# Kernel tuning notes

Measured on AMD Instinct MI355X. Metric: run time of the kernel, lower is better.

Reference implementation:

```python
import jax, jax.numpy as jnp
import numpy as np

G, S, D = 2, 1024, 2048   # dispatch_group_size, seq_len_per_chip, hidden_dim
E, K = 8, 2               # num_routed_experts, num_experts_per_tok


def setup_inputs() -> dict:
    key = jax.random.key(0)
    ks = jax.random.split(key, 10)
    scale = 1.0 / np.sqrt(D)
    return {
        "x": jax.random.normal(ks[0], (G, S, D), jnp.float32),
        "weights": jax.random.uniform(ks[1], (G, S, K), jnp.float32),
        "indices": jax.random.randint(ks[2], (G, S, K), 0, E, jnp.int64),
        "expert_offsets": jnp.zeros((G, E), jnp.int64),
        "expert_token_counts": jnp.zeros((G, E), jnp.int64),
        # routed expert weights stacked over experts; F.linear(x, W) = x @ W.T, W is [out,in]=[D,D]
        "gate_w": jax.random.normal(ks[3], (E, D, D), jnp.float32) * scale,
        "up_w": jax.random.normal(ks[4], (E, D, D), jnp.float32) * scale,
        "down_w": jax.random.normal(ks[5], (E, D, D), jnp.float32) * scale,
        "shared_gate_w": jax.random.normal(ks[6], (D, D), jnp.float32) * scale,
        "shared_up_w": jax.random.normal(ks[7], (D, D), jnpp_dummy) if False else jax.random.normal(ks[7], (D, D), jnp.float32) * scale,
        "shared_down_w": jax.random.normal(ks[8], (D, D), jnp.float32) * scale,
    }


def expert_ffn(x, gw, uw, dw):
    # SiLU-gated FFN: silu(x @ gw.T) * (x @ uw.T) @ dw.T
    gate = jnp.einsum("gsd,od->gso", x, gw)
    up = jnp.einsum("gsd,od->gso", x, uw)
    act = jax.nn.silu(gate) * up
    return jnp.einsum("gsa,oa->gso", act, dw)


def reference(x, weights, indices, expert_offsets, expert_token_counts,
              gate_w, up_w, down_w, shared_gate_w, shared_up_w, shared_down_w):
    x = x.astype(jnp.float32)
    # shared expert on original tokens
    shared_out = expert_ffn(x, shared_gate_w, shared_up_w, shared_down_w)  # [G,S,D]

    # routed experts: compute all E expert FFNs densely (small E), then gather top-k
    gate = jnp.einsum("gsd,eod->egso", x, gate_w)      # [E,G,S,D]
    up = jnp.einsum("gsd,eod->egso", x, up_w)
    act = jax.nn.silu(gate) * up
    all_out = jnp.einsum("egsa,eoa->egso", act, down_w)  # [E,G,S,D]

    per_tok = jnp.transpose(all_out, (1, 2, 0, 3))       # [G,S,E,D]
    combined = jnp.take_along_axis(per_tok, indices[..., None], axis=2)  # [G,S,K,D]
    routed_out = jnp.sum(combined * weights[..., None], axis=2)          # [G,S,D]

    return routed_out + shared_out
```

## Files before the change

### kernel.cpp

```cpp
#include <hip/hip_runtime.h>
#include <cstdint>
#include <cstddef>

#define DHID 2048
#define NEXP 8
#define NTOK 2048
#define NPAIR 4096
#define NROWS 6144
#define MAXTILES 55
#define DD ((size_t)DHID * DHID)

typedef __attribute__((ext_vector_type(8))) __bf16 bf16x8;
typedef __attribute__((ext_vector_type(4))) __bf16 bf16x4;
typedef __attribute__((ext_vector_type(4))) float f32x4;

typedef __attribute__((address_space(3))) void lds_void;
typedef __attribute__((address_space(1))) void gbl_void;

__device__ __forceinline__ void gload16(const void* g, void* l) {
  __builtin_amdgcn_global_load_lds((gbl_void*)g, (lds_void*)l, 16, 0, 0);
}

__global__ void route_kernel(const int* __restrict__ idx, const float* __restrict__ wts,
                             int* __restrict__ tok_id, float* __restrict__ tok_w,
                             int* __restrict__ dst_id,
                             int* __restrict__ cnts, int* __restrict__ offs,
                             int2* __restrict__ tiles) {
  __shared__ int c[NEXP];
  __shared__ int cur[NEXP];
  const int t = threadIdx.x;
  if (t < NEXP) c[t] = 0;
  __syncthreads();
  for (int p = t; p < NPAIR; p += 256) atomicAdd(&c[idx[p]], 1);
  __syncthreads();
  if (t == 0) {
    int run = 0;
    for (int e = 0; e < NEXP; ++e) { cur[e] = run; offs[e] = run; cnts[e] = c[e]; run += c[e]; }
    offs[NEXP] = NPAIR; cnts[NEXP] = NTOK;
    int nt = 0;
    for (int e = 0; e <= NEXP; ++e) {
      const int ce = (e < NEXP) ? c[e] : NTOK;
      for (int m0 = 0; m0 < ce; m0 += 128) { tiles[nt].x = e; tiles[nt].y = m0; ++nt; }
    }
    for (; nt < MAXTILES; ++nt) { tiles[nt].x = -1; tiles[nt].y = 0; }
  }
  __syncthreads();
  for (int p = t; p < NPAIR; p += 256) {
    const int e = idx[p];
    const int slot = atomicAdd(&cur[e], 1);
    tok_id[slot] = p >> 1;
    tok_w[slot] = wts[p];
    dst_id[slot] = p;
  }
  for (int i = t; i < NTOK; i += 256) {
    tok_id[NPAIR + i] = i; tok_w[NPAIR + i] = 1.0f; dst_id[NPAIR + i] = NPAIR + i;
  }
}

__global__ void cast_all_kernel(const f32x4* __restrict__ gw, const f32x4* __restrict__ sgw,
                                const f32x4* __restrict__ uw, const f32x4* __restrict__ suw,
                                const f32x4* __restrict__ dwn, const f32x4* __restrict__ sdw,
                                const f32x4* __restrict__ x, bf16x4* __restrict__ dst) {
  const size_t L4 = DD / 4;
  const size_t base = (size_t)blockIdx.x * 512 + threadIdx.x;
#pragma unroll
  for (int half = 0; half < 2; ++half) {
    const size_t f = base + (size_t)half * 256;
    size_t r = f;
    const f32x4* src;
    if (r < 8 * L4) { src = gw; }
    else if ((r -= 8 * L4) < L4) { src = sgw; }
    else if ((r -= L4) < 8 * L4) { src = uw; }
    else if ((r -= 8 * L4) < L4) { src = suw; }
    else if ((r -= L4) < 8 * L4) { src = dwn; }
    else if ((r -= 8 * L4) < L4) { src = sdw; }
    else { r -= L4; src = x; }
    const f32x4 a = __builtin_nontemporal_load(src + r);
    bf16x4 o;
    o[0] = (__bf16)a[0]; o[1] = (__bf16)a[1]; o[2] = (__bf16)a[2]; o[3] = (__bf16)a[3];
    dst[f] = o;
  }
}

__global__ __launch_bounds__(256, 3) void gateup_kernel(
    const __bf16* __restrict__ xb,
    const __bf16* __restrict__ wbg, const __bf16* __restrict__ wbu,
    __bf16* __restrict__ act,
    const int* __restrict__ tok_id,
    const int* __restrict__ cnts, const int* __restrict__ offs,
    const int2* __restrict__ tiles) {
  const int2 tl = tiles[blockIdx.y];
  const int e = tl.x;
  if (e < 0) return;
  const int m0 = tl.y;
  const int cnt = cnts[e];
  const int n0 = blockIdx.x * 64;
  const int off = offs[e];
  const __bf16* Bg = wbg + (size_t)e * DD;
  const __bf16* Bu = wbu + (size_t)e * DD;

  __shared__ __align__(16) char sA[128 * 64 * 2];
  __shared__ __align__(16) char sBg[64 * 64 * 2];
  __shared__ __align__(16) char sBu[64 * 64 * 2];

  const int tid = threadIdx.x;
  const int lane = tid & 63;
  const int wv = tid >> 6;
  const int mw = (wv >> 1) * 64;
  const int nw = (wv & 1) * 32;
  const int q4 = lane >> 4;
  const int ln = lane & 15;

  const int rbase = tid >> 3;
  const int part = (tid & 7) ^ (rbase & 7);

  const char* gA[4];
#pragma unroll
  for (int j = 0; j < 4; ++j) {
    int r = m0 + rbase + 32 * j;
    r = (r < cnt) ? r : (cnt - 1);
    gA[j] = (const char*)(xb + (size_t)tok_id[off + r] * DHID) + part * 16;
  }
  const char* gBg[2]; const char* gBu[2];
#pragma unroll
  for (int j = 0; j < 2; ++j) {
    gBg[j] = (const char*)(Bg + (size_t)(n0 + rbase + 32 * j) * DHID) + part * 16;
    gBu[j] = (const char*)(Bu + (size_t)(n0 + rbase + 32 * j) * DHID) + part * 16;
  }

  f32x4 accg[4][2], accu[4][2];
  const f32x4 vz = {0.f, 0.f, 0.f, 0.f};
#pragma unroll
  for (int i = 0; i < 4; ++i)
#pragma unroll
    for (int j = 0; j < 2; ++j) { accg[i][j] = vz; accu[i][j] = vz; }

  for (int kt = 0; kt < DHID; kt += 64) {
#pragma unroll
    for (int j = 0; j < 4; ++j)
      gload16(gA[j] + (size_t)kt * 2, sA + (tid + j * 256) * 16);
#pragma unroll
    for (int j = 0; j < 2; ++j) {
      gload16(gBg[j] + (size_t)kt * 2, sBg + (tid + j * 256) * 16);
      gload16(gBu[j] + (size_t)kt * 2, sBu + (tid + j * 256) * 16);
    }
    __syncthreads();

#pragma unroll
    for (int h = 0; h < 2; ++h) {
      bf16x8 af[4];
#pragma unroll
      for (int im = 0; im < 4; ++im) {
        const int r = mw + im * 16 + ln;
        af[im] = *(const bf16x8*)(sA + ((r * 8 + ((q4 + 4 * h) ^ (r & 7))) << 4));
      }
#pragma unroll
      for (int in_ = 0; in_ < 2; ++in_) {
        const int r = nw + in_ * 16 + ln;
        const int c = (r * 8 + ((q4 + 4 * h) ^ (r & 7))) << 4;
        const bf16x8 bg = *(const bf16x8*)(sBg + c);
        const bf16x8 bu = *(const bf16x8*)(sBu + c);
#pragma unroll
        for (int im = 0; im < 4; ++im) {
          accg[im][in_] = __builtin_amdgcn_mfma_f32_16x16x32_bf16(af[im], bg, accg[im][in_], 0, 0, 0);
          accu[im][in_] = __builtin_amdgcn_mfma_f32_16x16x32_bf16(af[im], bu, accu[im][in_], 0, 0, 0);
        }
      }
    }
    __syncthreads();
  }

#pragma unroll
  for (int im = 0; im < 4; ++im) {
#pragma unroll
    for (int rr = 0; rr < 4; ++rr) {
      const int row = mw + im * 16 + q4 * 4 + rr;
      if (m0 + row < cnt) {
        __bf16* dst = act + (size_t)(off + m0 + row) * DHID + n0 + nw + ln;
#pragma unroll
        for (int in_ = 0; in_ < 2; ++in_) {
          const float gg = accg[im][in_][rr];
          const float uu = accu[im][in_][rr];
          const float a = (gg / (1.0f + __expf(-gg))) * uu;
          dst[in_ * 16] = (__bf16)a;
        }
      }
    }
  }
}

__global__ __launch_bounds__(256, 3) void down_kernel(
    const __bf16* __restrict__ act,
    const __bf16* __restrict__ wbd,
    float* __restrict__ buf,
    const float* __restrict__ tok_w, const int* __restrict__ dst_id,
    const int* __restrict__ cnts, const int* __restrict__ offs,
    const int2* __restrict__ tiles) {
  const int2 tl = tiles[blockIdx.y];
  const int e = tl.x;
  if (e < 0) return;
  const int m0 = tl.y;
  const int cnt = cnts[e];
  const int n0 = blockIdx.x * 128;
  const int off = offs[e];
  const __bf16* B = wbd + (size_t)e * DD;

  __shared__ __align__(16) char sA[128 * 64 * 2];
  __shared__ __align__(16) char sB[128 * 64 * 2];

  const int tid = threadIdx.x;
  const int lane = tid & 63;
  const int wv = tid >> 6;
  const int mw = (wv >> 1) * 64;
  const int nw = (wv & 1) * 64;
  const int q4 = lane >> 4;
  const int ln = lane & 15;

  const int rbase = tid >> 3;
  const int part = (tid & 7) ^ (rbase & 7);

  const char* gA[4];
  const char* gB[4];
#pragma unroll
  for (int j = 0; j < 4; ++j) {
    gA[j] = (const char*)(act + (size_t)(off + m0 + rbase + 32 * j) * DHID) + part * 16;
    gB[j] = (const char*)(B + (size_t)(n0 + rbase + 32 * j) * DHID) + part * 16;
  }

  f32x4 acc[4][4];
  const f32x4 vz = {0.f, 0.f, 0.f, 0.f};
#pragma unroll
  for (int i = 0; i < 4; ++i)
#pragma unroll
    for (int j = 0; j < 4; ++j) acc[i][j] = vz;

  for (int kt = 0; kt < DHID; kt += 64) {
#pragma unroll
    for (int j = 0; j < 4; ++j) {
      gload16(gA[j] + (size_t)kt * 2, sA + (tid + j * 256) * 16);
      gload16(gB[j] + (size_t)kt * 2, sB + (tid + j * 256) * 16);
    }
    __syncthreads();

#pragma unroll
    for (int h = 0; h < 2; ++h) {
      bf16x8 af[4], bfr[4];
#pragma unroll
      for (int im = 0; im < 4; ++im) {
        const int r = mw + im * 16 + ln;
        af[im] = *(const bf16x8*)(sA + ((r * 8 + ((q4 + 4 * h) ^ (r & 7))) << 4));
      }
#pragma unroll
      for (int in_ = 0; in_ < 4; ++in_) {
        const int r = nw + in_ * 16 + ln;
        bfr[in_] = *(const bf16x8*)(sB + ((r * 8 + ((q4 + 4 * h) ^ (r & 7))) << 4));
      }
#pragma unroll
      for (int in_ = 0; in_ < 4; ++in_)
#pragma unroll
        for (int im = 0; im < 4; ++im)
          acc[im][in_] = __builtin_amdgcn_mfma_f32_16x16x32_bf16(af[im], bfr[in_], acc[im][in_], 0, 0, 0);
    }
    __syncthreads();
  }

#pragma unroll
  for (int im = 0; im < 4; ++im) {
#pragma unroll
    for (int rr = 0; rr < 4; ++rr) {
      const int row = mw + im * 16 + q4 * 4 + rr;
      if (m0 + row < cnt) {
        const int gr = off + m0 + row;
        const float wt = tok_w[gr];
        float* dst = buf + (size_t)dst_id[gr] * DHID + n0 + nw + ln;
#pragma unroll
        for (int in_ = 0; in_ < 4; ++in_)
          dst[in_ * 16] = wt * acc[im][in_][rr];
      }
    }
  }
}

__global__ void combine_kernel(const float4* __restrict__ buf, float4* __restrict__ out) {
  const int i = blockIdx.x * 256 + threadIdx.x;
  const int t = i >> 9;
  const int d = i & 511;
  const float4 a = buf[(size_t)(2 * t) * 512 + d];
  const float4 b = buf[(size_t)(2 * t + 1) * 512 + d];
  const float4 c = buf[(size_t)(NPAIR + t) * 512 + d];
  float4 r;
  r.x = a.x + b.x + c.x; r.y = a.y + b.y + c.y;
  r.z = a.z + b.z + c.z; r.w = a.w + b.w + c.w;
  out[i] = r;
}

extern "C" void kernel_launch(void* const* d_in, const int* in_sizes, int n_in,
                              void* d_out, int out_size, void* d_ws, size_t ws_size,
                              hipStream_t stream) {
  (void)in_sizes; (void)n_in; (void)out_size; (void)ws_size;
  const float* x   = (const float*)d_in[0];
  const float* wts = (const float*)d_in[1];
  const int*   idx = (const int*)d_in[2];
  const float* gw  = (const float*)d_in[5];
  const float* uw  = (const float*)d_in[6];
  const float* dwn = (const float*)d_in[7];
  const float* sgw = (const float*)d_in[8];
  const float* suw = (const float*)d_in[9];
  const float* sdw = (const float*)d_in[10];
  float* out = (float*)d_out;
  char* ws = (char*)d_ws;

  const size_t WB    = 3 * 9 * DD * 2;
  const size_t XBsz  = (size_t)NTOK * DHID * 2;
  const size_t ACTsz = (size_t)NROWS * DHID * 2;
  const size_t BUFsz = (size_t)NROWS * DHID * 4;

  __bf16* wbg = (__bf16*)ws;
  __bf16* wbu = wbg + 9 * DD;
  __bf16* wbd = wbu + 9 * DD;
  __bf16* xb  = (__bf16*)(ws + WB);
  __bf16* act = (__bf16*)(ws + WB + XBsz);
  float*  buf = (float*)(ws + WB + XBsz + ACTsz);
  char*   rt  = ws + WB + XBsz + ACTsz + BUFsz;
  int*   tok_id = (int*)rt;
  float* tok_w  = (float*)(rt + NROWS * 4);
  int*   dst_id = (int*)(rt + NROWS * 8);
  int*   cnts   = (int*)(rt + NROWS * 12);
  int*   offs   = cnts + 16;
  int2*  tiles  = (int2*)(offs + 16);

  route_kernel<<<1, 256, 0, stream>>>(idx, wts, tok_id, tok_w, dst_id, cnts, offs, tiles);
  cast_all_kernel<<<57344, 256, 0, stream>>>((const f32x4*)gw, (const f32x4*)sgw,
                                             (const f32x4*)uw, (const f32x4*)suw,
                                             (const f32x4*)dwn, (const f32x4*)sdw,
                                             (const f32x4*)x, (bf16x4*)ws);
  gateup_kernel<<<dim3(32, MAXTILES), 256, 0, stream>>>(
      xb, wbg, wbu, act, tok_id, cnts, offs, tiles);
  down_kernel<<<dim3(16, MAXTILES), 256, 0, stream>>>(
      act, wbd, buf, tok_w, dst_id, cnts, offs, tiles);
  combine_kernel<<<4096, 256, 0, stream>>>((const float4*)buf, (float4*)out);
}
```

Baseline: 608.0 us.

## Fuse routing into cast kernel and overlap down-weight cast with gate/up GEMM

```diff
diff --git a/kernel.cpp b/kernel.cpp
--- a/kernel.cpp
+++ b/kernel.cpp
@@ -8,6 +8,7 @@
 #define NPAIR 4096
 #define NROWS 6144
 #define MAXTILES 55
+#define CASTY 144
 #define DD ((size_t)DHID * DHID)
 
 typedef __attribute__((ext_vector_type(8))) __bf16 bf16x8;
@@ -21,64 +22,64 @@
   __builtin_amdgcn_global_load_lds((gbl_void*)g, (lds_void*)l, 16, 0, 0);
 }
 
-__global__ void route_kernel(const int* __restrict__ idx, const float* __restrict__ wts,
-                             int* __restrict__ tok_id, float* __restrict__ tok_w,
-                             int* __restrict__ dst_id,
-                             int* __restrict__ cnts, int* __restrict__ offs,
-                             int2* __restrict__ tiles) {
-  __shared__ int c[NEXP];
-  __shared__ int cur[NEXP];
-  const int t = threadIdx.x;
-  if (t < NEXP) c[t] = 0;
-  __syncthreads();
-  for (int p = t; p < NPAIR; p += 256) atomicAdd(&c[idx[p]], 1);
-  __syncthreads();
-  if (t == 0) {
-    int run = 0;
-    for (int e = 0; e < NEXP; ++e) { cur[e] = run; offs[e] = run; cnts[e] = c[e]; run += c[e]; }
-    offs[NEXP] = NPAIR; cnts[NEXP] = NTOK;
-    int nt = 0;
-    for (int e = 0; e <= NEXP; ++e) {
-      const int ce = (e < NEXP) ? c[e] : NTOK;
-      for (int m0 = 0; m0 < ce; m0 += 128) { tiles[nt].x = e; tiles[nt].y = m0; ++nt; }
-    }
-    for (; nt < MAXTILES; ++nt) { tiles[nt].x = -1; tiles[nt].y = 0; }
-  }
-  __syncthreads();
-  for (int p = t; p < NPAIR; p += 256) {
-    const int e = idx[p];
-    const int slot = atomicAdd(&cur[e], 1);
-    tok_id[slot] = p >> 1;
-    tok_w[slot] = wts[p];
-    dst_id[slot] = p;
-  }
-  for (int i = t; i < NTOK; i += 256) {
-    tok_id[NPAIR + i] = i; tok_w[NPAIR + i] = 1.0f; dst_id[NPAIR + i] = NPAIR + i;
-  }
-}
-
-__global__ void cast_all_kernel(const f32x4* __restrict__ gw, const f32x4* __restrict__ sgw,
-                                const f32x4* __restrict__ uw, const f32x4* __restrict__ suw,
-                                const f32x4* __restrict__ dwn, const f32x4* __restrict__ sdw,
-                                const f32x4* __restrict__ x, bf16x4* __restrict__ dst) {
+__global__ void cast_route_kernel(
+    const f32x4* __restrict__ gw, const f32x4* __restrict__ sgw,
+    const f32x4* __restrict__ uw, const f32x4* __restrict__ suw,
+    const f32x4* __restrict__ x, bf16x4* __restrict__ dst,
+    const int* __restrict__ idx, const float* __restrict__ wts,
+    int* __restrict__ tok_id, float* __restrict__ tok_w,
+    int* __restrict__ dst_id,
+    int* __restrict__ cnts, int* __restrict__ offs,
+    int2* __restrict__ tiles) {
+  if (blockIdx.x == 0) {
+    __shared__ int c[NEXP];
+    __shared__ int cur[NEXP];
+    const int t = threadIdx.x;
+    if (t < NEXP) c[t] = 0;
+    __syncthreads();
+    for (int p = t; p < NPAIR; p += 256) atomicAdd(&c[idx[p]], 1);
+    __syncthreads();
+    if (t == 0) {
+      int run = 0;
+      for (int e = 0; e < NEXP; ++e) { cur[e] = run; offs[e] = run; cnts[e] = c[e]; run += c[e]; }
+      offs[NEXP] = NPAIR; cnts[NEXP] = NTOK;
+      int nt = 0;
+      for (int e = 0; e <= NEXP; ++e) {
+        const int ce = (e < NEXP) ? c[e] : NTOK;
+        for (int m0 = 0; m0 < ce; m0 += 128) { tiles[nt].x = e; tiles[nt].y = m0; ++nt; }
+      }
+      for (; nt < MAXTILES; ++nt) { tiles[nt].x = -1; tiles[nt].y = 0; }
+    }
+    __syncthreads();
+    for (int p = t; p < NPAIR; p += 256) {
+      const int e = idx[p];
+      const int slot = atomicAdd(&cur[e], 1);
+      tok_id[slot] = p >> 1;
+      tok_w[slot] = wts[p];
+      dst_id[slot] = p;
+    }
+    for (int i = t; i < NTOK; i += 256) {
+      tok_id[NPAIR + i] = i; tok_w[NPAIR + i] = 1.0f; dst_id[NPAIR + i] = NPAIR + i;
+    }
+    return;
+  }
   const size_t L4 = DD / 4;
-  const size_t base = (size_t)blockIdx.x * 512 + threadIdx.x;
+  const size_t base = (size_t)(blockIdx.x - 1) * 512 + threadIdx.x;
 #pragma unroll
   for (int half = 0; half < 2; ++half) {
     const size_t f = base + (size_t)half * 256;
     size_t r = f;
+    size_t d = f;
     const f32x4* src;
     if (r < 8 * L4) { src = gw; }
     else if ((r -= 8 * L4) < L4) { src = sgw; }
     else if ((r -= L4) < 8 * L4) { src = uw; }
     else if ((r -= 8 * L4) < L4) { src = suw; }
-    else if ((r -= L4) < 8 * L4) { src = dwn; }
-    else if ((r -= 8 * L4) < L4) { src = sdw; }
-    else { r -= L4; src = x; }
+    else { r -= L4; src = x; d = 27 * L4 + r; }
     const f32x4 a = __builtin_nontemporal_load(src + r);
     bf16x4 o;
     o[0] = (__bf16)a[0]; o[1] = (__bf16)a[1]; o[2] = (__bf16)a[2]; o[3] = (__bf16)a[3];
-    dst[f] = o;
+    dst[d] = o;
   }
 }
 
@@ -88,7 +89,27 @@
     __bf16* __restrict__ act,
     const int* __restrict__ tok_id,
     const int* __restrict__ cnts, const int* __restrict__ offs,
-    const int2* __restrict__ tiles) {
+    const int2* __restrict__ tiles,
+    const f32x4* __restrict__ dwn, const f32x4* __restrict__ sdw,
+    bf16x4* __restrict__ castdst) {
+  if (blockIdx.y >= MAXTILES) {
+    const size_t L4 = DD / 4;
+    const int cb = (blockIdx.y - MAXTILES) * 32 + blockIdx.x;
+    const size_t base = (size_t)cb * 2048 + threadIdx.x;
+#pragma unroll
+    for (int j = 0; j < 8; ++j) {
+      const size_t f = base + (size_t)j * 256;
+      size_t r = f;
+      const f32x4* src = dwn;
+      if (r >= 8 * L4) { r -= 8 * L4; src = sdw; }
+      const f32x4 a = __builtin_nontemporal_load(src + r);
+      bf16x4 o;
+      o[0] = (__bf16)a[0]; o[1] = (__bf16)a[1]; o[2] = (__bf16)a[2]; o[3] = (__bf16)a[3];
+      castdst[18 * L4 + f] = o;
+    }
+    return;
+  }
+
   const int2 tl = tiles[blockIdx.y];
   const int e = tl.x;
   if (e < 0) return;
@@ -329,13 +350,13 @@
   int*   offs   = cnts + 16;
   int2*  tiles  = (int2*)(offs + 16);
 
-  route_kernel<<<1, 256, 0, stream>>>(idx, wts, tok_id, tok_w, dst_id, cnts, offs, tiles);
-  cast_all_kernel<<<57344, 256, 0, stream>>>((const f32x4*)gw, (const f32x4*)sgw,
-                                             (const f32x4*)uw, (const f32x4*)suw,
-                                             (const f32x4*)dwn, (const f32x4*)sdw,
-                                             (const f32x4*)x, (bf16x4*)ws);
-  gateup_kernel<<<dim3(32, MAXTILES), 256, 0, stream>>>(
-      xb, wbg, wbu, act, tok_id, cnts, offs, tiles);
+  cast_route_kernel<<<38913, 256, 0, stream>>>(
+      (const f32x4*)gw, (const f32x4*)sgw, (const f32x4*)uw, (const f32x4*)suw,
+      (const f32x4*)x, (bf16x4*)ws,
+      idx, wts, tok_id, tok_w, dst_id, cnts, offs, tiles);
+  gateup_kernel<<<dim3(32, MAXTILES + CASTY), 256, 0, stream>>>(
+      xb, wbg, wbu, act, tok_id, cnts, offs, tiles,
+      (const f32x4*)dwn, (const f32x4*)sdw, (bf16x4*)ws);
   down_kernel<<<dim3(16, MAXTILES), 256, 0, stream>>>(
       act, wbd, buf, tok_w, dst_id, cnts, offs, tiles);
   combine_kernel<<<4096, 256, 0, stream>>>((const float4*)buf, (float4*)out);
```

New measurement: 567.9 us. 6.6% less time.
